# Optimization experiments

Measured on AMD Instinct MI355X. Metric: run time of the kernel, lower is better.

The kernel has to match this reference:

```python
import jax, jax.numpy as jnp
import numpy as np

COMMITMENT_COST = 0.25
EPS = 1e-10


def setup_inputs() -> dict:
    key = jax.random.key(0)
    k1, k2 = jax.random.split(key)
    inputs = jax.random.normal(k1, (8192, 8, 8, 8, 8), dtype=jnp.float32)
    codebook = jax.random.normal(k2, (512, 4096), dtype=jnp.float32)  # [E, D]
    return {"inputs": inputs, "codebook": codebook}


def reference(inputs, codebook):
    input_shape = inputs.shape
    B = input_shape[0]
    E, D = codebook.shape
    flat = inputs.reshape(B, -1)  # [B, D], D == embedding_dim

    distances = (
        jnp.sum(flat * flat, axis=1, keepdims=True)
        + jnp.sum(codebook * codebook, axis=1)
        - 2.0 * jnp.matmul(flat, codebook.T)
    )  # [B, E]

    encoding_indices = jnp.argmin(distances, axis=1)  # [B]
    encodings = jax.nn.one_hot(encoding_indices, E, dtype=inputs.dtype)  # [B, E]

    # Gather quantize (same math as encodings @ codebook)
    quantized = jnp.take(codebook, encoding_indices, axis=0).reshape(input_shape)

    e_latent_loss = jnp.mean((jax.lax.stop_gradient(quantized) - inputs) ** 2)
    q_latent_loss = jnp.mean((quantized - jax.lax.stop_gradient(inputs)) ** 2)
    loss = q_latent_loss + COMMITMENT_COST * e_latent_loss

    # Straight-through estimator
    quantized_st = inputs + jax.lax.stop_gradient(quantized - inputs)

    avg_probs = jnp.mean(encodings, axis=0)  # [E]
    perplexity = jnp.exp(-jnp.sum(avg_probs * jnp.log(avg_probs + EPS)))

    return (loss, quantized_st, perplexity, encodings)
```

## Files before the change

kernel.cpp:

```cpp
#include <hip/hip_runtime.h>
#include <stdint.h>

#define B_ROWS 8192
#define DIM 4096
#define E_CODES 512
#define MARGIN 16.0f

typedef __attribute__((ext_vector_type(8))) short short8;
typedef __attribute__((ext_vector_type(4))) float floatx4;

#define WS_SCORES 0
#define WS_ENORM  4194304
#define WS_COUNTS 4194816
#define WS_LOSS   4195328

#define O_LOSS 0
#define O_Q    1
#define O_PERP 33554433
#define O_ENC  33554434

__global__ __launch_bounds__(64) void k_enorm(const float* __restrict__ cb, float* __restrict__ enorm) {
    const int e = blockIdx.x;
    const int lane = threadIdx.x;
    const float4* c4 = (const float4*)(cb + (size_t)e * DIM);
    float p = 0.f;
#pragma unroll
    for (int j = 0; j < 16; j++) {
        float4 v = c4[j * 64 + lane];
        p = fmaf(v.x, v.x, fmaf(v.y, v.y, fmaf(v.z, v.z, fmaf(v.w, v.w, p))));
    }
    for (int off = 32; off; off >>= 1) p += __shfl_down(p, off);
    if (lane == 0) enorm[e] = p;
}

__device__ inline uint32_t pk2(float hi, float lo) {
    return __builtin_amdgcn_perm(__float_as_uint(hi), __float_as_uint(lo), 0x07060302u);
}

#define LDK 56
__global__ __launch_bounds__(256) void k_gemm(const float* __restrict__ X, const float* __restrict__ CB,
                                              const float* __restrict__ enorm, float* __restrict__ scores) {
    __shared__ __align__(16) unsigned short As[128 * LDK];
    __shared__ __align__(16) unsigned short Bs[128 * LDK];
    const int bn = blockIdx.x & 3;
    const int bm = blockIdx.x >> 2;
    const int tid = threadIdx.x;
    const int lane = tid & 63;
    const int w = tid >> 6, wr = w >> 1, wc = w & 1;
    const int m16 = lane & 15, q4 = lane >> 4;
    const int r = tid >> 1;
    const int ko = (tid & 1) << 4;
    const float* xg = X + (size_t)(bm * 128 + r) * DIM + ko;
    const float* cg = CB + (size_t)(bn * 128 + r) * DIM + ko;

    floatx4 acc[4][4];
#pragma unroll
    for (int i = 0; i < 4; i++)
#pragma unroll
        for (int j = 0; j < 4; j++) acc[i][j] = (floatx4){0.f, 0.f, 0.f, 0.f};

    for (int kt = 0; kt < DIM; kt += 32) {
        const float4* xa = (const float4*)(xg + kt);
        const float4* ca = (const float4*)(cg + kt);
        float4 xv0 = xa[0], xv1 = xa[1], xv2 = xa[2], xv3 = xa[3];
        float4 cv0 = ca[0], cv1 = ca[1], cv2 = ca[2], cv3 = ca[3];
        __syncthreads();
        *(uint4*)(&As[r * LDK + ko])     = make_uint4(pk2(xv0.y, xv0.x), pk2(xv0.w, xv0.z), pk2(xv1.y, xv1.x), pk2(xv1.w, xv1.z));
        *(uint4*)(&As[r * LDK + ko + 8]) = make_uint4(pk2(xv2.y, xv2.x), pk2(xv2.w, xv2.z), pk2(xv3.y, xv3.x), pk2(xv3.w, xv3.z));
        *(uint4*)(&Bs[r * LDK + ko])     = make_uint4(pk2(cv0.y, cv0.x), pk2(cv0.w, cv0.z), pk2(cv1.y, cv1.x), pk2(cv1.w, cv1.z));
        *(uint4*)(&Bs[r * LDK + ko + 8]) = make_uint4(pk2(cv2.y, cv2.x), pk2(cv2.w, cv2.z), pk2(cv3.y, cv3.x), pk2(cv3.w, cv3.z));
        __syncthreads();
        short8 a[4], b[4];
#pragma unroll
        for (int f = 0; f < 4; f++) {
            a[f] = *(const short8*)(&As[(wr * 64 + f * 16 + m16) * LDK + q4 * 8]);
            b[f] = *(const short8*)(&Bs[(wc * 64 + f * 16 + m16) * LDK + q4 * 8]);
        }
#pragma unroll
        for (int i = 0; i < 4; i++)
#pragma unroll
            for (int j = 0; j < 4; j++)
                acc[i][j] = __builtin_amdgcn_mfma_f32_16x16x32_bf16(a[i], b[j], acc[i][j], 0, 0, 0);
    }

#pragma unroll
    for (int fc = 0; fc < 4; fc++) {
        const int col = bn * 128 + wc * 64 + fc * 16 + m16;
        const float en = enorm[col];
#pragma unroll
        for (int fr = 0; fr < 4; fr++) {
            const int row0 = bm * 128 + wr * 64 + fr * 16 + q4 * 4;
#pragma unroll
            for (int rr = 0; rr < 4; rr++)
                scores[(size_t)(row0 + rr) * E_CODES + col] = en - 2.0f * acc[fr][fc][rr];
        }
    }
}

__global__ __launch_bounds__(256) void k_fused(const float* __restrict__ X, const float* __restrict__ CB,
                                               const float* __restrict__ scores, int* __restrict__ counts,
                                               float* __restrict__ loss_sum, float* __restrict__ out) {
    const int row = blockIdx.x;
    const int tid = threadIdx.x;
    const int lane = tid & 63, w = tid >> 6;
    __shared__ float redv[4];
    __shared__ int redi[4];
    __shared__ int cand[64];
    __shared__ int ncand;

    float s0 = scores[(size_t)row * E_CODES + tid];
    float s1 = scores[(size_t)row * E_CODES + 256 + tid];
    if (tid == 0) ncand = 0;

    float mv; int mi;
    if (s1 < s0) { mv = s1; mi = tid + 256; } else { mv = s0; mi = tid; }
    for (int off = 32; off; off >>= 1) {
        float ov = __shfl_down(mv, off);
        int   oi = __shfl_down(mi, off);
        if (ov < mv || (ov == mv && oi < mi)) { mv = ov; mi = oi; }
    }
    if (lane == 0) { redv[w] = mv; redi[w] = mi; }
    __syncthreads();
    if (tid == 0) {
        for (int k = 1; k < 4; k++)
            if (redv[k] < redv[0] || (redv[k] == redv[0] && redi[k] < redi[0])) { redv[0] = redv[k]; redi[0] = redi[k]; }
    }
    __syncthreads();
    const float thr = redv[0] + MARGIN;

    if (s0 <= thr) { int p = atomicAdd(&ncand, 1); if (p < 64) cand[p] = tid; }
    if (s1 <= thr) { int p = atomicAdd(&ncand, 1); if (p < 64) cand[p] = tid + 256; }
    __syncthreads();
    const int nc = min(ncand, 64);

    const float* xr = X + (size_t)row * DIM;
    float bestd = 3.0e38f; int beste = 1 << 30;
    for (int c = 0; c < nc; c++) {
        const int e = cand[c];
        const float* cr = CB + (size_t)e * DIM;
        float p = 0.f;
#pragma unroll
        for (int j = 0; j < 16; j++) {
            const int idx = j * 256 + tid;
            const float d = xr[idx] - cr[idx];
            p = fmaf(d, d, p);
        }
        for (int off = 32; off; off >>= 1) p += __shfl_down(p, off);
        __syncthreads();
        if (lane == 0) redv[w] = p;
        __syncthreads();
        const float dist = ((redv[0] + redv[1]) + redv[2]) + redv[3];
        if (dist < bestd || (dist == bestd && e < beste)) { bestd = dist; beste = e; }
    }

    const float* cq = CB + (size_t)beste * DIM;
    float* oq = out + O_Q + (size_t)row * DIM;
#pragma unroll
    for (int j = 0; j < 16; j++) {
        const int idx = j * 256 + tid;
        const float x = xr[idx];
        const float q = cq[idx];
        oq[idx] = x + (q - x);
    }
    float* oe = out + O_ENC + (size_t)row * E_CODES;
    oe[tid]       = (tid == beste) ? 1.0f : 0.0f;
    oe[tid + 256] = (tid + 256 == beste) ? 1.0f : 0.0f;
    if (tid == 0) {
        atomicAdd(&counts[beste], 1);
        atomicAdd(loss_sum, bestd);
    }
}

__global__ __launch_bounds__(512) void k_final(const int* __restrict__ counts, const float* __restrict__ loss_sum,
                                               float* __restrict__ out) {
    const int tid = threadIdx.x;
    const int lane = tid & 63, w = tid >> 6;
    __shared__ float r[8];
    const float p = (float)counts[tid] * (1.0f / 8192.0f);
    float h = p * logf(p + 1e-10f);
    for (int off = 32; off; off >>= 1) h += __shfl_down(h, off);
    if (lane == 0) r[w] = h;
    __syncthreads();
    if (tid == 0) {
        float H = 0.f;
        for (int k = 0; k < 8; k++) H += r[k];
        out[O_PERP] = expf(-H);
        out[O_LOSS] = loss_sum[0] * (1.25f / 33554432.0f);
    }
}

extern "C" void kernel_launch(void* const* d_in, const int* in_sizes, int n_in,
                              void* d_out, int out_size, void* d_ws, size_t ws_size,
                              hipStream_t stream) {
    const float* X  = (const float*)d_in[0];
    const float* CB = (const float*)d_in[1];
    float* out = (float*)d_out;
    float* ws  = (float*)d_ws;
    float* scores = ws + WS_SCORES;
    float* enorm  = ws + WS_ENORM;
    int*   counts = (int*)(ws + WS_COUNTS);
    float* loss_s = ws + WS_LOSS;

    hipMemsetAsync(counts, 0, (E_CODES + 1) * sizeof(int), stream);

    k_enorm<<<E_CODES, 64, 0, stream>>>(CB, enorm);
    k_gemm<<<256, 256, 0, stream>>>(X, CB, enorm, scores);
    k_fused<<<B_ROWS, 256, 0, stream>>>(X, CB, scores, counts, loss_s, out);
    k_final<<<1, 512, 0, stream>>>(counts, loss_s, out);
}
```

Before: 511.1 us.

## Retile GEMM to 64x128 blocks and process one row per wavefront in fused kernel

The GEMM now uses 64x128 tiles with 512 threads and a K-step of 64, launching 512 blocks instead of 256 so more of the GPU's compute units are busy. The fused argmin/refine kernel assigns one row per wavefront instead of one row per block. Each wavefront keeps its input row in registers, finds candidates with ballot masks and reduces with shuffles, which removes shared-memory and __syncthreads reductions. It also uses vectorized float4/float2 loads and stores. Costs are higher register pressure from holding 16 float4 per lane, and lower MFMA reuse per tile.

```diff
diff --git a/kernel.cpp b/kernel.cpp
--- a/kernel.cpp
+++ b/kernel.cpp
@@ -8,6 +8,7 @@
 
 typedef __attribute__((ext_vector_type(8))) short short8;
 typedef __attribute__((ext_vector_type(4))) float floatx4;
+typedef __attribute__((ext_vector_type(4), aligned(4))) float f4u;
 
 #define WS_SCORES 0
 #define WS_ENORM  4194304
@@ -37,62 +38,66 @@
     return __builtin_amdgcn_perm(__float_as_uint(hi), __float_as_uint(lo), 0x07060302u);
 }
 
-#define LDK 56
-__global__ __launch_bounds__(256) void k_gemm(const float* __restrict__ X, const float* __restrict__ CB,
+#define LDK 72
+__global__ __launch_bounds__(512) void k_gemm(const float* __restrict__ X, const float* __restrict__ CB,
                                               const float* __restrict__ enorm, float* __restrict__ scores) {
-    __shared__ __align__(16) unsigned short As[128 * LDK];
+    __shared__ __align__(16) unsigned short As[64 * LDK];
     __shared__ __align__(16) unsigned short Bs[128 * LDK];
+    const int bm = blockIdx.x >> 2;
     const int bn = blockIdx.x & 3;
-    const int bm = blockIdx.x >> 2;
     const int tid = threadIdx.x;
     const int lane = tid & 63;
-    const int w = tid >> 6, wr = w >> 1, wc = w & 1;
+    const int w = tid >> 6, wr = w >> 2, wc = w & 3;
     const int m16 = lane & 15, q4 = lane >> 4;
-    const int r = tid >> 1;
-    const int ko = (tid & 1) << 4;
-    const float* xg = X + (size_t)(bm * 128 + r) * DIM + ko;
-    const float* cg = CB + (size_t)(bn * 128 + r) * DIM + ko;
-
-    floatx4 acc[4][4];
-#pragma unroll
-    for (int i = 0; i < 4; i++)
-#pragma unroll
-        for (int j = 0; j < 4; j++) acc[i][j] = (floatx4){0.f, 0.f, 0.f, 0.f};
-
-    for (int kt = 0; kt < DIM; kt += 32) {
+
+    const int rA = tid >> 3, cA = (tid & 7) * 8;
+    const int rB = tid >> 2, cB = (tid & 3) * 16;
+    const float* xg = X + (size_t)(bm * 64 + rA) * DIM + cA;
+    const float* cg = CB + (size_t)(bn * 128 + rB) * DIM + cB;
+
+    floatx4 acc[2][2];
+#pragma unroll
+    for (int i = 0; i < 2; i++)
+#pragma unroll
+        for (int j = 0; j < 2; j++) acc[i][j] = (floatx4){0.f, 0.f, 0.f, 0.f};
+
+    for (int kt = 0; kt < DIM; kt += 64) {
         const float4* xa = (const float4*)(xg + kt);
         const float4* ca = (const float4*)(cg + kt);
-        float4 xv0 = xa[0], xv1 = xa[1], xv2 = xa[2], xv3 = xa[3];
+        float4 xv0 = xa[0], xv1 = xa[1];
         float4 cv0 = ca[0], cv1 = ca[1], cv2 = ca[2], cv3 = ca[3];
         __syncthreads();
-        *(uint4*)(&As[r * LDK + ko])     = make_uint4(pk2(xv0.y, xv0.x), pk2(xv0.w, xv0.z), pk2(xv1.y, xv1.x), pk2(xv1.w, xv1.z));
-        *(uint4*)(&As[r * LDK + ko + 8]) = make_uint4(pk2(xv2.y, xv2.x), pk2(xv2.w, xv2.z), pk2(xv3.y, xv3.x), pk2(xv3.w, xv3.z));
-        *(uint4*)(&Bs[r * LDK + ko])     = make_uint4(pk2(cv0.y, cv0.x), pk2(cv0.w, cv0.z), pk2(cv1.y, cv1.x), pk2(cv1.w, cv1.z));
-        *(uint4*)(&Bs[r * LDK + ko + 8]) = make_uint4(pk2(cv2.y, cv2.x), pk2(cv2.w, cv2.z), pk2(cv3.y, cv3.x), pk2(cv3.w, cv3.z));
+        *(uint4*)(&As[rA * LDK + cA]) = make_uint4(pk2(xv0.y, xv0.x), pk2(xv0.w, xv0.z), pk2(xv1.y, xv1.x), pk2(xv1.w, xv1.z));
+        *(uint4*)(&Bs[rB * LDK + cB])     = make_uint4(pk2(cv0.y, cv0.x), pk2(cv0.w, cv0.z), pk2(cv1.y, cv1.x), pk2(cv1.w, cv1.z));
+        *(uint4*)(&Bs[rB * LDK + cB + 8]) = make_uint4(pk2(cv2.y, cv2.x), pk2(cv2.w, cv2.z), pk2(cv3.y, cv3.x), pk2(cv3.w, cv3.z));
         __syncthreads();
-        short8 a[4], b[4];
-#pragma unroll
-        for (int f = 0; f < 4; f++) {
-            a[f] = *(const short8*)(&As[(wr * 64 + f * 16 + m16) * LDK + q4 * 8]);
-            b[f] = *(const short8*)(&Bs[(wc * 64 + f * 16 + m16) * LDK + q4 * 8]);
-        }
-#pragma unroll
-        for (int i = 0; i < 4; i++)
-#pragma unroll
-            for (int j = 0; j < 4; j++)
-                acc[i][j] = __builtin_amdgcn_mfma_f32_16x16x32_bf16(a[i], b[j], acc[i][j], 0, 0, 0);
-    }
-
-#pragma unroll
-    for (int fc = 0; fc < 4; fc++) {
-        const int col = bn * 128 + wc * 64 + fc * 16 + m16;
+        short8 a[2][2], b[2][2];
+#pragma unroll
+        for (int i = 0; i < 2; i++)
+#pragma unroll
+            for (int kk = 0; kk < 2; kk++) {
+                a[i][kk] = *(const short8*)(&As[(wr * 32 + i * 16 + m16) * LDK + kk * 32 + q4 * 8]);
+                b[i][kk] = *(const short8*)(&Bs[(wc * 32 + i * 16 + m16) * LDK + kk * 32 + q4 * 8]);
+            }
+#pragma unroll
+        for (int kk = 0; kk < 2; kk++)
+#pragma unroll
+            for (int i = 0; i < 2; i++)
+#pragma unroll
+                for (int j = 0; j < 2; j++)
+                    acc[i][j] = __builtin_amdgcn_mfma_f32_16x16x32_bf16(a[i][kk], b[j][kk], acc[i][j], 0, 0, 0);
+    }
+
+#pragma unroll
+    for (int j = 0; j < 2; j++) {
+        const int col = bn * 128 + wc * 32 + j * 16 + m16;
         const float en = enorm[col];
 #pragma unroll
-        for (int fr = 0; fr < 4; fr++) {
-            const int row0 = bm * 128 + wr * 64 + fr * 16 + q4 * 4;
+        for (int i = 0; i < 2; i++) {
+            const int row0 = bm * 64 + wr * 32 + i * 16 + q4 * 4;
 #pragma unroll
             for (int rr = 0; rr < 4; rr++)
-                scores[(size_t)(row0 + rr) * E_CODES + col] = en - 2.0f * acc[fr][fc][rr];
+                scores[(size_t)(row0 + rr) * E_CODES + col] = en - 2.0f * acc[i][j][rr];
         }
     }
 }
@@ -100,72 +105,69 @@
 __global__ __launch_bounds__(256) void k_fused(const float* __restrict__ X, const float* __restrict__ CB,
                                                const float* __restrict__ scores, int* __restrict__ counts,
                                                float* __restrict__ loss_sum, float* __restrict__ out) {
-    const int row = blockIdx.x;
     const int tid = threadIdx.x;
     const int lane = tid & 63, w = tid >> 6;
-    __shared__ float redv[4];
-    __shared__ int redi[4];
-    __shared__ int cand[64];
-    __shared__ int ncand;
-
-    float s0 = scores[(size_t)row * E_CODES + tid];
-    float s1 = scores[(size_t)row * E_CODES + 256 + tid];
-    if (tid == 0) ncand = 0;
-
-    float mv; int mi;
-    if (s1 < s0) { mv = s1; mi = tid + 256; } else { mv = s0; mi = tid; }
+    const int row = blockIdx.x * 4 + w;
+
+    const float* sr = scores + (size_t)row * E_CODES;
+    float s[8];
+#pragma unroll
+    for (int g = 0; g < 8; g++) s[g] = sr[g * 64 + lane];
+
+    float mv = s[0]; int mi = lane;
+#pragma unroll
+    for (int g = 1; g < 8; g++) { if (s[g] < mv) { mv = s[g]; mi = g * 64 + lane; } }
     for (int off = 32; off; off >>= 1) {
-        float ov = __shfl_down(mv, off);
-        int   oi = __shfl_down(mi, off);
+        float ov = __shfl_xor(mv, off); int oi = __shfl_xor(mi, off);
         if (ov < mv || (ov == mv && oi < mi)) { mv = ov; mi = oi; }
     }
-    if (lane == 0) { redv[w] = mv; redi[w] = mi; }
-    __syncthreads();
-    if (tid == 0) {
-        for (int k = 1; k < 4; k++)
-            if (redv[k] < redv[0] || (redv[k] == redv[0] && redi[k] < redi[0])) { redv[0] = redv[k]; redi[0] = redi[k]; }
-    }
-    __syncthreads();
-    const float thr = redv[0] + MARGIN;
-
-    if (s0 <= thr) { int p = atomicAdd(&ncand, 1); if (p < 64) cand[p] = tid; }
-    if (s1 <= thr) { int p = atomicAdd(&ncand, 1); if (p < 64) cand[p] = tid + 256; }
-    __syncthreads();
-    const int nc = min(ncand, 64);
-
-    const float* xr = X + (size_t)row * DIM;
+    const float thr = mv + MARGIN;
+
+    const float4* xr4 = (const float4*)(X + (size_t)row * DIM);
+    float4 xv[16];
+#pragma unroll
+    for (int i = 0; i < 16; i++) xv[i] = xr4[i * 64 + lane];
+
     float bestd = 3.0e38f; int beste = 1 << 30;
-    for (int c = 0; c < nc; c++) {
-        const int e = cand[c];
-        const float* cr = CB + (size_t)e * DIM;
-        float p = 0.f;
-#pragma unroll
-        for (int j = 0; j < 16; j++) {
-            const int idx = j * 256 + tid;
-            const float d = xr[idx] - cr[idx];
-            p = fmaf(d, d, p);
+#pragma unroll 1
+    for (int g = 0; g < 8; g++) {
+        unsigned long long mask = __ballot(s[g] <= thr);
+        while (mask) {
+            const int b = __builtin_ctzll(mask); mask &= mask - 1;
+            const int e = g * 64 + b;
+            const float4* cr4 = (const float4*)(CB + (size_t)e * DIM);
+            float p = 0.f;
+#pragma unroll
+            for (int i = 0; i < 16; i++) {
+                float4 c = cr4[i * 64 + lane];
+                float dx = xv[i].x - c.x, dy = xv[i].y - c.y, dz = xv[i].z - c.z, dw = xv[i].w - c.w;
+                p = fmaf(dx, dx, fmaf(dy, dy, fmaf(dz, dz, fmaf(dw, dw, p))));
+            }
+            for (int off = 32; off; off >>= 1) p += __shfl_xor(p, off);
+            if (p < bestd || (p == bestd && e < beste)) { bestd = p; beste = e; }
         }
-        for (int off = 32; off; off >>= 1) p += __shfl_down(p, off);
-        __syncthreads();
-        if (lane == 0) redv[w] = p;
-        __syncthreads();
-        const float dist = ((redv[0] + redv[1]) + redv[2]) + redv[3];
-        if (dist < bestd || (dist == bestd && e < beste)) { bestd = dist; beste = e; }
-    }
-
-    const float* cq = CB + (size_t)beste * DIM;
-    float* oq = out + O_Q + (size_t)row * DIM;
-#pragma unroll
-    for (int j = 0; j < 16; j++) {
-        const int idx = j * 256 + tid;
-        const float x = xr[idx];
-        const float q = cq[idx];
-        oq[idx] = x + (q - x);
-    }
-    float* oe = out + O_ENC + (size_t)row * E_CODES;
-    oe[tid]       = (tid == beste) ? 1.0f : 0.0f;
-    oe[tid + 256] = (tid + 256 == beste) ? 1.0f : 0.0f;
-    if (tid == 0) {
+    }
+
+    const float4* cq4 = (const float4*)(CB + (size_t)beste * DIM);
+    f4u* oq4 = (f4u*)(out + O_Q + (size_t)row * DIM);
+#pragma unroll
+    for (int i = 0; i < 16; i++) {
+        float4 x = xv[i], q = cq4[i * 64 + lane];
+        f4u r;
+        r.x = x.x + (q.x - x.x); r.y = x.y + (q.y - x.y);
+        r.z = x.z + (q.z - x.z); r.w = x.w + (q.w - x.w);
+        oq4[i * 64 + lane] = r;
+    }
+
+    float2* oe2 = (float2*)(out + O_ENC + (size_t)row * E_CODES);
+#pragma unroll
+    for (int k = 0; k < 4; k++) {
+        const int e0 = (k * 64 + lane) * 2;
+        float2 v; v.x = (e0 == beste) ? 1.0f : 0.0f; v.y = (e0 + 1 == beste) ? 1.0f : 0.0f;
+        oe2[k * 64 + lane] = v;
+    }
+
+    if (lane == 0) {
         atomicAdd(&counts[beste], 1);
         atomicAdd(loss_sum, bestd);
     }
@@ -204,7 +206,7 @@
     hipMemsetAsync(counts, 0, (E_CODES + 1) * sizeof(int), stream);
 
     k_enorm<<<E_CODES, 64, 0, stream>>>(CB, enorm);
-    k_gemm<<<256, 256, 0, stream>>>(X, CB, enorm, scores);
-    k_fused<<<B_ROWS, 256, 0, stream>>>(X, CB, scores, counts, loss_s, out);
+    k_gemm<<<512, 512, 0, stream>>>(X, CB, enorm, scores);
+    k_fused<<<B_ROWS / 4, 256, 0, stream>>>(X, CB, scores, counts, loss_s, out);
     k_final<<<1, 512, 0, stream>>>(counts, loss_s, out);
 }
```

Result: faster. 468.1 us (-8.4%).
